# Optimization experiments

Hardware: AMD Instinct MI355X
Metric: run time of the kernel (lower is better)

The kernel has to match this reference:

```python
import jax, jax.numpy as jnp
import numpy as np

B, K, N_ANN, C = 8, 100000, 32, 80
ALPHA, GAMMA = 0.25, 0.5


def setup_inputs() -> dict:
    key = jax.random.key(0)
    k1, k2, k3, k4, k5, k6, k7 = jax.random.split(key, 7)
    classifications = jax.random.uniform(k1, (B, K, C), jnp.float32, 0.01, 0.99)
    regressions = jax.random.normal(k2, (B, K, 4), jnp.float32)
    # anchors: valid boxes (x1,y1,x2,y2) on a ~1024px image
    a_ctr = jax.random.uniform(k3, (1, K, 2), jnp.float32, 32.0, 992.0)
    a_wh = jax.random.uniform(k4, (1, K, 2), jnp.float32, 16.0, 256.0)
    anchors = jnp.concatenate([a_ctr - a_wh / 2, a_ctr + a_wh / 2], axis=-1)
    # GT annotations: (x1,y1,x2,y2,label), all valid (label >= 0)
    g_ctr = jax.random.uniform(k5, (B, N_ANN, 2), jnp.float32, 64.0, 960.0)
    g_wh = jax.random.uniform(k6, (B, N_ANN, 2), jnp.float32, 16.0, 256.0)
    labels = jax.random.randint(k7, (B, N_ANN, 1), 0, C).astype(jnp.float32)
    annotations = jnp.concatenate([g_ctr - g_wh / 2, g_ctr + g_wh / 2, labels], axis=-1)
    return {"classifications": classifications, "regressions": regressions,
            "anchors": anchors, "annotations": annotations}


def _calc_iou(a, b):
    # a: [K,4] anchors, b: [N,4] gt boxes -> IoU [K,N]
    area_b = (b[:, 2] - b[:, 0]) * (b[:, 3] - b[:, 1])
    area_a = (a[:, 2] - a[:, 0]) * (a[:, 3] - a[:, 1])
    iw = jnp.clip(jnp.minimum(a[:, None, 2], b[None, :, 2]) - jnp.maximum(a[:, None, 0], b[None, :, 0]), 0.0)
    ih = jnp.clip(jnp.minimum(a[:, None, 3], b[None, :, 3]) - jnp.maximum(a[:, None, 1], b[None, :, 1]), 0.0)
    inter = iw * ih
    union = jnp.clip(area_a[:, None] + area_b[None, :] - inter, 1e-8)
    return inter / union


def _per_image(classification, regression, annotation, anchor):
    p = jnp.clip(classification, 1e-4, 1.0 - 1e-4)
    valid = annotation[:, 4] >= 0  # label == -1 means padding
    iou = _calc_iou(anchor, annotation[:, :4])                  # [K,N]
    iou = jnp.where(valid[None, :], iou, -1.0)
    iou_max = jnp.max(iou, axis=1)                               # [K]
    iou_argmax = jnp.argmax(iou, axis=1)                         # [K]
    positive = iou_max >= 0.5                                    # [K]
    num_pos = jnp.sum(positive.astype(jnp.float32))

    assigned = annotation[iou_argmax]                            # [K,5]
    onehot = jax.nn.one_hot(assigned[:, 4].astype(jnp.int32), C, dtype=p.dtype)  # [K,C]
    # targets: -1 = ignore, 0 = negative, 1 = matched class
    base = jnp.where(iou_max < 0.4, 0.0, -1.0)[:, None]          # [K,1]
    targets = jnp.where(positive[:, None], onehot, base)         # [K,C]

    is_pos_cls = targets == 1.0
    alpha_factor = jnp.where(is_pos_cls, ALPHA, 1.0 - ALPHA)
    focal_weight = alpha_factor * jnp.where(is_pos_cls, 1.0 - p, p) ** GAMMA
    bce = -(targets * jnp.log(p) + (1.0 - targets) * jnp.log(1.0 - p))
    cls_loss = jnp.where(targets != -1.0, focal_weight * bce, 0.0)
    cls_loss = jnp.sum(cls_loss) / jnp.clip(num_pos, 1.0)

    aw = anchor[:, 2] - anchor[:, 0]
    ah = anchor[:, 3] - anchor[:, 1]
    acx = anchor[:, 0] + 0.5 * aw
    acy = anchor[:, 1] + 0.5 * ah
    gw = jnp.clip(assigned[:, 2] - assigned[:, 0], 1.0)
    gh = jnp.clip(assigned[:, 3] - assigned[:, 1], 1.0)
    gcx = assigned[:, 0] + 0.5 * gw
    gcy = assigned[:, 1] + 0.5 * gh
    t = jnp.stack([(gcx - acx) / aw, (gcy - acy) / ah, jnp.log(gw / aw), jnp.log(gh / ah)], axis=1)
    t = t / jnp.array([0.1, 0.1, 0.2, 0.2], dtype=t.dtype)
    diff = jnp.abs(t - regression)                               # [K,4]
    sl1 = jnp.where(diff <= 1.0 / 9.0, 0.5 * 9.0 * diff * diff, diff - 0.5 / 9.0)
    reg_sum = jnp.sum(jnp.where(positive[:, None], sl1, 0.0))
    reg_loss = jnp.where(num_pos > 0, reg_sum / jnp.clip(num_pos * 4.0, 1.0), 0.0)
    return cls_loss, reg_loss


def reference(classifications, regressions, anchors, annotations):
    anchor = anchors[0]
    cls_losses, reg_losses = jax.vmap(_per_image, in_axes=(0, 0, 0, None))(
        classifications, regressions, annotations, anchor)
    # original returns mean over batch (keepdim); pack both scalars into [2]
    return jnp.stack([jnp.mean(cls_losses), jnp.mean(reg_losses)])
```

## Files before the change

kernel.cpp:

```cpp
#include <hip/hip_runtime.h>
#include <math.h>

#define B_ 8
#define K_ 100000
#define NANN 32
#define C_ 80
#define BLOCK 256
#define LN2 0.69314718056f

#define WS_M_OFF 32

__global__ void zero_ws_kernel(float* ws) {
    int i = threadIdx.x;
    if (i < 3 * B_) ws[i] = 0.0f;
}

__device__ __forceinline__ float fast_log2(float x) {
#if __has_builtin(__builtin_amdgcn_logf)
    return __builtin_amdgcn_logf(x);
#else
    return __log2f(x);
#endif
}
__device__ __forceinline__ float fast_sqrt(float x) {
#if __has_builtin(__builtin_amdgcn_sqrtf)
    return __builtin_amdgcn_sqrtf(x);
#else
    return sqrtf(x);
#endif
}

__launch_bounds__(BLOCK)
__global__ void focal_assign(const float* __restrict__ cls,
                             const float* __restrict__ reg,
                             const float* __restrict__ anc,
                             const float* __restrict__ ann,
                             float* __restrict__ ws) {
    const int b   = blockIdx.y;
    const int tid = threadIdx.x;
    const int k   = blockIdx.x * BLOCK + tid;

    __shared__ float s_ann[NANN * 5];
    __shared__ float s_red[(BLOCK / 64) * 3];

    if (tid < NANN * 5) s_ann[tid] = ann[b * NANN * 5 + tid];
    __syncthreads();

    float reg_acc  = 0.0f;
    float np_acc   = 0.0f;
    float cls_corr = 0.0f;
    float m        = 0.0f;

    if (k < K_) {
        float4 a = *(const float4*)(anc + (size_t)k * 4);
        float aw = a.z - a.x, ah = a.w - a.y;
        float area_a = aw * ah;

        float best = -2.0f;
        int bestj = 0;
        for (int j = 0; j < NANN; ++j) {
            float bx1 = s_ann[j * 5 + 0], by1 = s_ann[j * 5 + 1];
            float bx2 = s_ann[j * 5 + 2], by2 = s_ann[j * 5 + 3];
            float lbl = s_ann[j * 5 + 4];
            float area_b = (bx2 - bx1) * (by2 - by1);
            float iw = fmaxf(fminf(a.z, bx2) - fmaxf(a.x, bx1), 0.0f);
            float ih = fmaxf(fminf(a.w, by2) - fmaxf(a.y, by1), 0.0f);
            float inter = iw * ih;
            float uni = fmaxf(area_a + area_b - inter, 1e-8f);
            float iou = inter / uni;
            if (lbl < 0.0f) iou = -1.0f;
            if (iou > best) { best = iou; bestj = j; }
        }

        if (best >= 0.5f) {
            m = 1.0f;
            np_acc = 1.0f;
            int c = (int)s_ann[bestj * 5 + 4];
            float p  = cls[((size_t)b * K_ + k) * C_ + c];
            float pm = 1.0f - p;
            float pos_term = -0.25f * fast_sqrt(pm) * (fast_log2(p)  * LN2);
            float neg_term = -0.75f * fast_sqrt(p)  * (fast_log2(pm) * LN2);
            cls_corr = pos_term - neg_term;

            float gx1 = s_ann[bestj * 5 + 0], gy1 = s_ann[bestj * 5 + 1];
            float gx2 = s_ann[bestj * 5 + 2], gy2 = s_ann[bestj * 5 + 3];
            float gw = fmaxf(gx2 - gx1, 1.0f);
            float gh = fmaxf(gy2 - gy1, 1.0f);
            float gcx = gx1 + 0.5f * gw, gcy = gy1 + 0.5f * gh;
            float acx = a.x + 0.5f * aw, acy = a.y + 0.5f * ah;
            float4 r = *(const float4*)(reg + ((size_t)b * K_ + k) * 4);
            float t0 = ((gcx - acx) / aw) * 10.0f;
            float t1 = ((gcy - acy) / ah) * 10.0f;
            float t2 = (fast_log2(gw / aw) * LN2) * 5.0f;
            float t3 = (fast_log2(gh / ah) * LN2) * 5.0f;
            float d, s;
            d = fabsf(t0 - r.x); s = (d <= 1.0f/9.0f) ? 4.5f*d*d : d - 0.5f/9.0f; reg_acc += s;
            d = fabsf(t1 - r.y); s = (d <= 1.0f/9.0f) ? 4.5f*d*d : d - 0.5f/9.0f; reg_acc += s;
            d = fabsf(t2 - r.z); s = (d <= 1.0f/9.0f) ? 4.5f*d*d : d - 0.5f/9.0f; reg_acc += s;
            d = fabsf(t3 - r.w); s = (d <= 1.0f/9.0f) ? 4.5f*d*d : d - 0.5f/9.0f; reg_acc += s;
        } else if (best < 0.4f) {
            m = 1.0f;
        }

        ws[WS_M_OFF + (size_t)b * K_ + k] = m;
    }

    float v0 = cls_corr, v1 = reg_acc, v2 = np_acc;
    for (int off = 32; off > 0; off >>= 1) {
        v0 += __shfl_down(v0, off, 64);
        v1 += __shfl_down(v1, off, 64);
        v2 += __shfl_down(v2, off, 64);
    }
    int wave = tid >> 6, lane = tid & 63;
    if (lane == 0) {
        s_red[wave * 3 + 0] = v0;
        s_red[wave * 3 + 1] = v1;
        s_red[wave * 3 + 2] = v2;
    }
    __syncthreads();
    if (tid == 0) {
        float c = 0.0f, rg = 0.0f, np = 0.0f;
        for (int w = 0; w < BLOCK / 64; ++w) {
            c  += s_red[w * 3 + 0];
            rg += s_red[w * 3 + 1];
            np += s_red[w * 3 + 2];
        }
        atomicAdd(&ws[b * 3 + 0], c);
        atomicAdd(&ws[b * 3 + 1], rg);
        atomicAdd(&ws[b * 3 + 2], np);
    }
}

#define SWEEP_GX 256
#define NF4 (K_ * C_ / 4)
#define MLP 8

__launch_bounds__(BLOCK, 4)
__global__ void focal_sweep(const float* __restrict__ cls,
                            const float* __restrict__ ws_m,
                            float* __restrict__ ws) {
    const int b   = blockIdx.y;
    const int tid = threadIdx.x;
    const unsigned S  = SWEEP_GX * BLOCK;
    unsigned g = blockIdx.x * BLOCK + tid;

    const float4* __restrict__ cp = (const float4*)(cls + (size_t)b * K_ * C_);
    const float*  __restrict__ mb = ws_m + (size_t)b * K_;

    float a0 = 0.0f, a1 = 0.0f, a2 = 0.0f, a3 = 0.0f;

    for (; g + (MLP - 1) * S < (unsigned)NF4; g += MLP * S) {
        float4 x[MLP];
        float  mm[MLP];
#pragma unroll
        for (int i = 0; i < MLP; ++i) {
            unsigned gi = g + i * S;
            x[i]  = cp[gi];
            mm[i] = mb[gi / 20u];
        }
#pragma unroll
        for (int i = 0; i < MLP; ++i) {
            a0 = fmaf(mm[i], fast_sqrt(x[i].x) * fast_log2(1.0f - x[i].x), a0);
            a1 = fmaf(mm[i], fast_sqrt(x[i].y) * fast_log2(1.0f - x[i].y), a1);
            a2 = fmaf(mm[i], fast_sqrt(x[i].z) * fast_log2(1.0f - x[i].z), a2);
            a3 = fmaf(mm[i], fast_sqrt(x[i].w) * fast_log2(1.0f - x[i].w), a3);
        }
    }
    for (; g < (unsigned)NF4; g += S) {
        float4 x = cp[g];
        float mm = mb[g / 20u];
        a0 = fmaf(mm, fast_sqrt(x.x) * fast_log2(1.0f - x.x), a0);
        a1 = fmaf(mm, fast_sqrt(x.y) * fast_log2(1.0f - x.y), a1);
        a2 = fmaf(mm, fast_sqrt(x.z) * fast_log2(1.0f - x.z), a2);
        a3 = fmaf(mm, fast_sqrt(x.w) * fast_log2(1.0f - x.w), a3);
    }

    float cls_acc = ((a0 + a1) + (a2 + a3)) * (-0.75f * LN2);

    __shared__ float s_red[BLOCK / 64];
    for (int off = 32; off > 0; off >>= 1)
        cls_acc += __shfl_down(cls_acc, off, 64);
    int wave = tid >> 6, lane = tid & 63;
    if (lane == 0) s_red[wave] = cls_acc;
    __syncthreads();
    if (tid == 0) {
        float c = 0.0f;
        for (int w = 0; w < BLOCK / 64; ++w) c += s_red[w];
        atomicAdd(&ws[b * 3 + 0], c);
    }
}

__global__ void finalize_kernel(const float* __restrict__ ws, float* __restrict__ out) {
    if (threadIdx.x == 0) {
        float cs = 0.0f, rs = 0.0f;
        for (int b = 0; b < B_; ++b) {
            float c  = ws[b * 3 + 0];
            float r  = ws[b * 3 + 1];
            float np = ws[b * 3 + 2];
            cs += c / fmaxf(np, 1.0f);
            rs += (np > 0.0f) ? r / fmaxf(np * 4.0f, 1.0f) : 0.0f;
        }
        out[0] = cs / (float)B_;
        out[1] = rs / (float)B_;
    }
}

extern "C" void kernel_launch(void* const* d_in, const int* in_sizes, int n_in,
                              void* d_out, int out_size, void* d_ws, size_t ws_size,
                              hipStream_t stream) {
    const float* cls = (const float*)d_in[0];
    const float* reg = (const float*)d_in[1];
    const float* anc = (const float*)d_in[2];
    const float* ann = (const float*)d_in[3];
    float* out = (float*)d_out;
    float* ws  = (float*)d_ws;

    zero_ws_kernel<<<1, 64, 0, stream>>>(ws);

    dim3 g1((K_ + BLOCK - 1) / BLOCK, B_);
    focal_assign<<<g1, BLOCK, 0, stream>>>(cls, reg, anc, ann, ws);

    dim3 g2(SWEEP_GX, B_);
    focal_sweep<<<g2, BLOCK, 0, stream>>>(cls, ws + WS_M_OFF, ws);

    finalize_kernel<<<1, 64, 0, stream>>>(ws, out);
}
```

Before: 452.7 us.

## Sweep all anchors unmasked first, subtract ignored-anchor rows in assign kernel

The sweep kernel no longer reads a per-anchor mask. It sums the negative focal term over every classification element, using one-shot slabs of 2000 float4 per block, and it now runs before the assign kernel. The assign kernel then subtracts the full-row contribution for anchors in the ignore band (IoU between 0.4 and 0.5), which removes the mask write and read traffic and the integer divide per element. The cost is an extra 80-float row read for each ignored anchor, and a float cancellation that may change accumulation precision.

Result: slower. 463.3 us (+2.3%).

```diff
diff --git a/kernel.cpp b/kernel.cpp
--- a/kernel.cpp
+++ b/kernel.cpp
@@ -8,8 +8,6 @@
 #define BLOCK 256
 #define LN2 0.69314718056f
 
-#define WS_M_OFF 32
-
 __global__ void zero_ws_kernel(float* ws) {
     int i = threadIdx.x;
     if (i < 3 * B_) ws[i] = 0.0f;
@@ -28,6 +26,48 @@
 #else
     return sqrtf(x);
 #endif
+}
+
+#define SLAB 2000
+#define SW_GX 1000
+
+__launch_bounds__(BLOCK, 4)
+__global__ void focal_sweep(const float* __restrict__ cls,
+                            float* __restrict__ ws) {
+    const int b   = blockIdx.y;
+    const int tid = threadIdx.x;
+    const float4* __restrict__ cp =
+        (const float4*)(cls + (size_t)b * (K_ * C_)) + (size_t)blockIdx.x * SLAB;
+
+    float4 x[8];
+#pragma unroll
+    for (int j = 0; j < 8; ++j) {
+        x[j] = make_float4(0.0f, 0.0f, 0.0f, 0.0f);
+        int idx = j * BLOCK + tid;
+        if (idx < SLAB) x[j] = cp[idx];
+    }
+
+    float a0 = 0.0f, a1 = 0.0f, a2 = 0.0f, a3 = 0.0f;
+#pragma unroll
+    for (int j = 0; j < 8; ++j) {
+        a0 += fast_sqrt(x[j].x) * fast_log2(1.0f - x[j].x);
+        a1 += fast_sqrt(x[j].y) * fast_log2(1.0f - x[j].y);
+        a2 += fast_sqrt(x[j].z) * fast_log2(1.0f - x[j].z);
+        a3 += fast_sqrt(x[j].w) * fast_log2(1.0f - x[j].w);
+    }
+    float v = ((a0 + a1) + (a2 + a3)) * (-0.75f * LN2);
+
+    __shared__ float s_red[BLOCK / 64];
+    for (int off = 32; off > 0; off >>= 1)
+        v += __shfl_down(v, off, 64);
+    int wave = tid >> 6, lane = tid & 63;
+    if (lane == 0) s_red[wave] = v;
+    __syncthreads();
+    if (tid == 0) {
+        float c = 0.0f;
+        for (int w = 0; w < BLOCK / 64; ++w) c += s_red[w];
+        atomicAdd(&ws[b * 3 + 0], c);
+    }
 }
 
 __launch_bounds__(BLOCK)
@@ -49,7 +89,6 @@
     float reg_acc  = 0.0f;
     float np_acc   = 0.0f;
     float cls_corr = 0.0f;
-    float m        = 0.0f;
 
     if (k < K_) {
         float4 a = *(const float4*)(anc + (size_t)k * 4);
@@ -73,7 +112,6 @@
         }
 
         if (best >= 0.5f) {
-            m = 1.0f;
             np_acc = 1.0f;
             int c = (int)s_ann[bestj * 5 + 4];
             float p  = cls[((size_t)b * K_ + k) * C_ + c];
@@ -98,11 +136,20 @@
             d = fabsf(t1 - r.y); s = (d <= 1.0f/9.0f) ? 4.5f*d*d : d - 0.5f/9.0f; reg_acc += s;
             d = fabsf(t2 - r.z); s = (d <= 1.0f/9.0f) ? 4.5f*d*d : d - 0.5f/9.0f; reg_acc += s;
             d = fabsf(t3 - r.w); s = (d <= 1.0f/9.0f) ? 4.5f*d*d : d - 0.5f/9.0f; reg_acc += s;
-        } else if (best < 0.4f) {
-            m = 1.0f;
-        }
-
-        ws[WS_M_OFF + (size_t)b * K_ + k] = m;
+        } else if (best >= 0.4f) {
+            const float4* __restrict__ rp =
+                (const float4*)(cls + ((size_t)b * K_ + k) * C_);
+            float r0 = 0.0f, r1 = 0.0f, r2 = 0.0f, r3 = 0.0f;
+#pragma unroll
+            for (int j = 0; j < C_ / 4; ++j) {
+                float4 x = rp[j];
+                r0 += fast_sqrt(x.x) * fast_log2(1.0f - x.x);
+                r1 += fast_sqrt(x.y) * fast_log2(1.0f - x.y);
+                r2 += fast_sqrt(x.z) * fast_log2(1.0f - x.z);
+                r3 += fast_sqrt(x.w) * fast_log2(1.0f - x.w);
+            }
+            cls_corr = (0.75f * LN2) * ((r0 + r1) + (r2 + r3));
+        }
     }
 
     float v0 = cls_corr, v1 = reg_acc, v2 = np_acc;
@@ -128,65 +175,6 @@
         atomicAdd(&ws[b * 3 + 0], c);
         atomicAdd(&ws[b * 3 + 1], rg);
         atomicAdd(&ws[b * 3 + 2], np);
-    }
-}
-
-#define SWEEP_GX 256
-#define NF4 (K_ * C_ / 4)
-#define MLP 8
-
-__launch_bounds__(BLOCK, 4)
-__global__ void focal_sweep(const float* __restrict__ cls,
-                            const float* __restrict__ ws_m,
-                            float* __restrict__ ws) {
-    const int b   = blockIdx.y;
-    const int tid = threadIdx.x;
-    const unsigned S  = SWEEP_GX * BLOCK;
-    unsigned g = blockIdx.x * BLOCK + tid;
-
-    const float4* __restrict__ cp = (const float4*)(cls + (size_t)b * K_ * C_);
-    const float*  __restrict__ mb = ws_m + (size_t)b * K_;
-
-    float a0 = 0.0f, a1 = 0.0f, a2 = 0.0f, a3 = 0.0f;
-
-    for (; g + (MLP - 1) * S < (unsigned)NF4; g += MLP * S) {
-        float4 x[MLP];
-        float  mm[MLP];
-#pragma unroll
-        for (int i = 0; i < MLP; ++i) {
-            unsigned gi = g + i * S;
-            x[i]  = cp[gi];
-            mm[i] = mb[gi / 20u];
-        }
-#pragma unroll
-        for (int i = 0; i < MLP; ++i) {
-            a0 = fmaf(mm[i], fast_sqrt(x[i].x) * fast_log2(1.0f - x[i].x), a0);
-            a1 = fmaf(mm[i], fast_sqrt(x[i].y) * fast_log2(1.0f - x[i].y), a1);
-            a2 = fmaf(mm[i], fast_sqrt(x[i].z) * fast_log2(1.0f - x[i].z), a2);
-            a3 = fmaf(mm[i], fast_sqrt(x[i].w) * fast_log2(1.0f - x[i].w), a3);
-        }
-    }
-    for (; g < (unsigned)NF4; g += S) {
-        float4 x = cp[g];
-        float mm = mb[g / 20u];
-        a0 = fmaf(mm, fast_sqrt(x.x) * fast_log2(1.0f - x.x), a0);
-        a1 = fmaf(mm, fast_sqrt(x.y) * fast_log2(1.0f - x.y), a1);
-        a2 = fmaf(mm, fast_sqrt(x.z) * fast_log2(1.0f - x.z), a2);
-        a3 = fmaf(mm, fast_sqrt(x.w) * fast_log2(1.0f - x.w), a3);
-    }
-
-    float cls_acc = ((a0 + a1) + (a2 + a3)) * (-0.75f * LN2);
-
-    __shared__ float s_red[BLOCK / 64];
-    for (int off = 32; off > 0; off >>= 1)
-        cls_acc += __shfl_down(cls_acc, off, 64);
-    int wave = tid >> 6, lane = tid & 63;
-    if (lane == 0) s_red[wave] = cls_acc;
-    __syncthreads();
-    if (tid == 0) {
-        float c = 0.0f;
-        for (int w = 0; w < BLOCK / 64; ++w) c += s_red[w];
-        atomicAdd(&ws[b * 3 + 0], c);
     }
 }
 
@@ -217,11 +205,11 @@
 
     zero_ws_kernel<<<1, 64, 0, stream>>>(ws);
 
+    dim3 g2(SW_GX, B_);
+    focal_sweep<<<g2, BLOCK, 0, stream>>>(cls, ws);
+
     dim3 g1((K_ + BLOCK - 1) / BLOCK, B_);
     focal_assign<<<g1, BLOCK, 0, stream>>>(cls, reg, anc, ann, ws);
 
-    dim3 g2(SWEEP_GX, B_);
-    focal_sweep<<<g2, BLOCK, 0, stream>>>(cls, ws + WS_M_OFF, ws);
-
     finalize_kernel<<<1, 64, 0, stream>>>(ws, out);
 }
```
